# Kernel optimization log

Measured on AMD Instinct MI355X. Metric: run time of the kernel, lower is better.

The kernel has to match this reference:

```python
import jax, jax.numpy as jnp
import numpy as np

# Config (matches init_kwargs)
T, B = 128, 32
I, H, O, G = 128, 320, 32, 8
GROUP = 16  # attn_group_size entries, 8 groups of 16 -> sums to I
DT, TAU_X, TAU_W = 0.02, 0.1, 0.2
ALPHA_X = DT / TAU_X          # 0.2
ALPHA_W = DT / TAU_W          # 0.1
E_PROP = 0.8


def _masks():
    e_h = int(E_PROP * H)  # 256
    # x2h: e_prop=1, zero_cols_prop=0, no diag removal -> all ones
    mask_x = jnp.ones((H, I), dtype=jnp.float32)
    # h2h: sign mask (+1 for E, -1 for I), diagonal zeroed
    sign_h = jnp.concatenate([jnp.ones(e_h), -jnp.ones(H - e_h)]).astype(jnp.float32)
    mask_h = jnp.tile(sign_h[None, :], (H, 1)) * (1.0 - jnp.eye(H, dtype=jnp.float32))
    # h2o: zero_cols = int(0.2*H) trailing columns removed, sign mask on the rest
    zc = int((1.0 - E_PROP) * H)  # 64
    exist = jnp.concatenate([jnp.ones(H - zc), jnp.zeros(zc)]).astype(jnp.float32)
    mask_o = jnp.tile((sign_h * exist)[None, :], (O, 1))
    # attn EILinear(H -> G): same column pattern as h2o
    mask_a = jnp.tile((sign_h * exist)[None, :], (G, 1))
    return mask_x, mask_h, mask_o, mask_a


def setup_inputs() -> dict:
    key = jax.random.key(0)
    ks = jax.random.split(key, 10)
    s = 0.05  # keep dynamics in a sane range
    return {
        "x": jax.random.normal(ks[0], (T, B, I), dtype=jnp.float32),
        "Rs": jax.random.uniform(ks[1], (T, B, 1), dtype=jnp.float32),
        "W_x2h": jax.random.normal(ks[2], (H, I), dtype=jnp.float32) * s,
        "W_h2h": jax.random.normal(ks[3], (H, H), dtype=jnp.float32) * s,
        "b_h2h": jax.random.normal(ks[4], (H,), dtype=jnp.float32) * s,
        "W_h2o": jax.random.normal(ks[5], (O, H), dtype=jnp.float32) * s,
        "b_h2o": jax.random.normal(ks[6], (O,), dtype=jnp.float32) * s,
        "W_attn": jax.random.normal(ks[7], (G, H), dtype=jnp.float32) * s,
        "b_attn": jax.random.normal(ks[8], (G,), dtype=jnp.float32) * s,
        "c_plas": jax.random.normal(ks[9], (6,), dtype=jnp.float32) * s,
    }


def reference(x, Rs, W_x2h, W_h2h, b_h2h, W_h2o, b_h2o, W_attn, b_attn, c_plas):
    mask_x, mask_h, mask_o, mask_a = _masks()
    relu = jax.nn.relu
    # effective (sign/existence constrained, positive) weights
    ew_attn = relu(W_attn) * mask_a                      # [G, H]
    ew_x0 = relu(W_x2h) * mask_x                         # [H, I]
    ew_h0 = relu(W_h2h) * mask_h                         # [H, H]
    c = jnp.abs(c_plas)

    state0 = jnp.zeros((B, H), dtype=x.dtype)            # x0=0, sigma_rec=0
    output0 = relu(state0)
    wx0 = jnp.broadcast_to(ew_x0[None], (B, H, I))       # batched fast weights
    wh0 = jnp.broadcast_to(ew_h0[None], (B, H, H))

    def step(carry, inp):
        state, output, wx, wh = carry
        x_t, R_t = inp                                   # [B,I], [B,1]
        # attention over hidden groups
        attn = jax.nn.softmax(output @ ew_attn.T + b_attn, axis=-1)  # [B,G]
        attn_full = jnp.repeat(attn, GROUP, axis=-1)     # [B,I]
        xm = x_t * attn_full * G
        # masked / positive-constrained fast weights applied per batch
        ewx = relu(wx) * mask_x[None]                    # [B,H,I]
        ewh = relu(wh) * mask_h[None]                    # [B,H,H]
        total = (jnp.einsum('bhi,bi->bh', ewx, xm)
                 + jnp.einsum('bhj,bj->bh', ewh, output) + b_h2h)
        new_state = state * (1.0 - ALPHA_X) + total * ALPHA_X
        new_output = jnp.tanh(relu(new_state))           # retanh
        # outer-product plasticity update
        R = R_t[:, :, None]                              # [B,1,1]
        wx_n = wx * (1.0 - ALPHA_W) + ALPHA_W * R * (
            c[0] * xm[:, None, :]
            + c[1] * new_output[:, :, None]
            + c[2] * jnp.einsum('bi,bj->bij', new_output, xm))
        wh_n = wh * (1.0 - ALPHA_W) + ALPHA_W * R * (
            c[3] * output[:, None, :]
            + c[4] * new_output[:, :, None]
            + c[5] * jnp.einsum('bi,bj->bij', new_output, output))
        return (new_state, new_output, wx_n, wh_n), new_output

    _, hs = jax.lax.scan(step, (state0, output0, wx0, wh0), (x, Rs))  # hs: [T,B,H]
    ew_o = relu(W_h2o) * mask_o                          # [O,H]
    out = jax.nn.sigmoid(jnp.einsum('tbh,oh->tbo', hs, ew_o) + b_h2o)
    return out, hs
```

## Files before the change

kernel.cpp:

```cpp
#include <hip/hip_runtime.h>

#define TT 128
#define BB 32
#define II 128
#define HH 320
#define OO 32
#define GG 8
#define HPAD 129

static __device__ __forceinline__ float fexp2(float x) { return __builtin_amdgcn_exp2f(x); }
static __device__ __forceinline__ float frcp(float x)  { return __builtin_amdgcn_rcpf(x); }

static __device__ __forceinline__ float tanh_pos(float x) {
    float e = fexp2(x * 2.8853900817779268f);
    return 1.0f - 2.0f * frcp(e + 1.0f);
}

__global__ __launch_bounds__(512, 2)
void leaky_rnn_kernel(const float* __restrict__ x, const float* __restrict__ Rs,
                      const float* __restrict__ Wx2h, const float* __restrict__ Wh2h,
                      const float* __restrict__ bh2h, const float* __restrict__ Wh2o,
                      const float* __restrict__ bh2o, const float* __restrict__ Wattn,
                      const float* __restrict__ battn, const float* __restrict__ cplas,
                      float* __restrict__ out, float* __restrict__ hs,
                      unsigned* __restrict__ ctr)
{
    const int tid  = threadIdx.x;
    const int bid  = blockIdx.x;
    const int b    = bid >> 3;
    const int sub  = bid & 7;
    const int w    = tid >> 6;
    const int lane = tid & 63;
    const int h0   = sub * 40;

    __shared__ float s_ea[GG * HH];
    __shared__ float s_out[2][HH];
    __shared__ float s_logit[GG];
    __shared__ float s_hist[40 * HPAD];
    __shared__ float s_hs[16 * HH];

    for (int idx = tid; idx < GG * HH; idx += 512) {
        int h = idx % HH;
        float m = (h < 256) ? 1.f : (h == 256 ? -1.f : 0.f);
        s_ea[idx] = fmaxf(Wattn[idx], 0.f) * m;
    }
    if (tid < HH) { s_out[0][tid] = 0.f; s_out[1][tid] = 0.f; }

    float wx[5][2], wh[5][5], st[5], bh[5];
    int hrow[5];
#pragma unroll
    for (int r = 0; r < 5; ++r) {
        int h = h0 + w * 5 + r;
        hrow[r] = h;
        bh[r] = bh2h[h];
        st[r] = 0.f;
#pragma unroll
        for (int c = 0; c < 2; ++c)
            wx[r][c] = fmaxf(Wx2h[h * II + lane + 64 * c], 0.f);
#pragma unroll
        for (int c = 0; c < 5; ++c) {
            int j = lane + 64 * c;
            float v = fmaxf(Wh2h[h * HH + j], 0.f);
            v = (c == 4) ? -v : v;
            wh[r][c] = (j == h) ? 0.f : v;
        }
    }
    float batt = battn[w];
    float c0 = fabsf(cplas[0]), c1 = fabsf(cplas[1]), c2 = fabsf(cplas[2]);
    float c3 = fabsf(cplas[3]), c4 = fabsf(cplas[4]), c5 = fabsf(cplas[5]);

    const float AX  = (float)(0.02 / 0.1);
    const float AW  = (float)(0.02 / 0.2);
    const float OMX = 1.f - AX;
    const float OMW = 1.f - AW;
    const float L2E = 1.4426950408889634f;

    __syncthreads();

    float xv0n = x[b * II + lane];
    float xv1n = x[b * II + lane + 64];
    float Rvn  = Rs[b];

#pragma unroll 1
    for (int t = 0; t < TT; ++t) {
        const float* so_cur = s_out[t & 1];
        float*       so_nxt = s_out[(t + 1) & 1];
        float xv0 = xv0n, xv1 = xv1n;
        float A   = AW * Rvn;

        float lp = 0.f;
#pragma unroll
        for (int k = 0; k < 5; ++k) {
            int hh2 = lane + 64 * k;
            lp = fmaf(s_ea[w * HH + hh2], so_cur[hh2], lp);
        }
#pragma unroll
        for (int m = 1; m < 64; m <<= 1) lp += __shfl_xor(lp, m, 64);
        if (lane == 0) s_logit[w] = lp + batt;
        __syncthreads();

        float lg[8];
#pragma unroll
        for (int g = 0; g < 8; ++g) lg[g] = s_logit[g];
        float mx = lg[0];
#pragma unroll
        for (int g = 1; g < 8; ++g) mx = fmaxf(mx, lg[g]);
        float se = 0.f, eg[8];
#pragma unroll
        for (int g = 0; g < 8; ++g) { eg[g] = fexp2((lg[g] - mx) * L2E); se += eg[g]; }
        float rinv = frcp(se);
        float xmc0 = xv0 * eg[lane >> 4] * 8.f * rinv;
        float xmc1 = xv1 * eg[(lane >> 4) + 4] * 8.f * rinv;

        float oc[5];
#pragma unroll
        for (int c = 0; c < 5; ++c) oc[c] = so_cur[lane + 64 * c];

        float p[5];
#pragma unroll
        for (int r = 0; r < 5; ++r) {
            int h = hrow[r];
            float pp = fmaxf(wx[r][0], 0.f) * xmc0;
            pp = fmaf(fmaxf(wx[r][1], 0.f), xmc1, pp);
#pragma unroll
            for (int c = 0; c < 5; ++c) {
                float wv = fmaxf(wh[r][c], 0.f);
                float so = (c == 4) ? -oc[4] : oc[c];
                float term = wv * so;
                term = ((lane + 64 * c) == h) ? 0.f : term;
                pp += term;
            }
            p[r] = pp;
        }
#pragma unroll
        for (int m = 1; m < 64; m <<= 1) {
#pragma unroll
            for (int r = 0; r < 5; ++r) p[r] += __shfl_xor(p[r], m, 64);
        }

        float no[5];
#pragma unroll
        for (int r = 0; r < 5; ++r) {
            float total = p[r] + bh[r];
            st[r] = fmaf(st[r], OMX, total * AX);
            no[r] = tanh_pos(fmaxf(st[r], 0.f));
        }

        {
            float pub = no[0];
            pub = (lane == 1) ? no[1] : pub;
            pub = (lane == 2) ? no[2] : pub;
            pub = (lane == 3) ? no[3] : pub;
            pub = (lane == 4) ? no[4] : pub;
            if (lane < 5) {
                __hip_atomic_store(&hs[(t * BB + b) * HH + h0 + w * 5 + lane], pub + 2.0f,
                                   __ATOMIC_RELAXED, __HIP_MEMORY_SCOPE_AGENT);
                s_hist[(w * 5 + lane) * HPAD + t] = pub;
            }
        }

        if (t < TT - 1) {
            float Ac0 = A * c0, Ac1 = A * c1, Ac2 = A * c2;
            float Ac3 = A * c3, Ac4 = A * c4, Ac5 = A * c5;
#pragma unroll
            for (int r = 0; r < 5; ++r) {
                float u  = fmaf(Ac2, no[r], Ac0);
                float v  = Ac1 * no[r];
                float pp = fmaf(Ac5, no[r], Ac3);
                float qq = Ac4 * no[r];
                wx[r][0] = fmaf(wx[r][0], OMW, fmaf(u, xmc0, v));
                wx[r][1] = fmaf(wx[r][1], OMW, fmaf(u, xmc1, v));
#pragma unroll
                for (int c = 0; c < 5; ++c)
                    wh[r][c] = fmaf(wh[r][c], OMW, fmaf(pp, oc[c], qq));
            }
        }

        if (t + 1 < TT) {
            xv0n = x[((t + 1) * BB + b) * II + lane];
            xv1n = x[((t + 1) * BB + b) * II + lane + 64];
            Rvn  = Rs[(t + 1) * BB + b];
        }

        if (t < TT - 1 && tid < HH) {
            const float* p2 = &hs[(t * BB + b) * HH + tid];
            float v; int guard = 0;
            do {
                v = __hip_atomic_load(p2, __ATOMIC_RELAXED, __HIP_MEMORY_SCOPE_AGENT);
            } while (v < 1.0f && ++guard < 2000000);
            so_nxt[tid] = v - 2.0f;
        }
        __syncthreads();
    }

    if (tid == 0) {
        __hip_atomic_fetch_add(&ctr[b * 32], 1u, __ATOMIC_RELAXED, __HIP_MEMORY_SCOPE_AGENT);
        int guard = 0;
        while (__hip_atomic_load(&ctr[b * 32], __ATOMIC_RELAXED, __HIP_MEMORY_SCOPE_AGENT) < 8u) {
            if (++guard > 2000000) break;
            __builtin_amdgcn_s_sleep(1);
        }
    }
    __syncthreads();

    for (int idx = tid; idx < 16 * HH; idx += 512) {
        int tl = idx / HH, h = idx % HH;
        int t_g = sub * 16 + tl;
        s_hs[idx] = __hip_atomic_load(&hs[(t_g * BB + b) * HH + h],
                                      __ATOMIC_RELAXED, __HIP_MEMORY_SCOPE_AGENT) - 2.0f;
    }
    __syncthreads();
    {
        int t_loc = tid >> 5;
        int o     = tid & 31;
        int t_g   = sub * 16 + t_loc;
        const float* hp = &s_hs[t_loc * HH];
        float acc = bh2o[o];
#pragma unroll 4
        for (int h = 0; h < 257; ++h) {
            float m = (h == 256) ? -1.f : 1.f;
            acc = fmaf(fmaxf(Wh2o[o * HH + h], 0.f) * m, hp[h], acc);
        }
        float sg = frcp(1.f + fexp2(-acc * L2E));
        out[(t_g * BB + b) * OO + o] = sg;
    }

    __syncthreads();
    if (tid == 0) {
        __hip_atomic_fetch_add(&ctr[b * 32], 1u, __ATOMIC_RELAXED, __HIP_MEMORY_SCOPE_AGENT);
        int guard = 0;
        while (__hip_atomic_load(&ctr[b * 32], __ATOMIC_RELAXED, __HIP_MEMORY_SCOPE_AGENT) < 16u) {
            if (++guard > 2000000) break;
            __builtin_amdgcn_s_sleep(1);
        }
    }
    __syncthreads();

    for (int idx = tid; idx < 40 * TT; idx += 512) {
        int row = idx >> 7;
        int t   = idx & 127;
        __hip_atomic_store(&hs[(t * BB + b) * HH + h0 + row], s_hist[row * HPAD + t],
                           __ATOMIC_RELAXED, __HIP_MEMORY_SCOPE_AGENT);
    }
}

extern "C" void kernel_launch(void* const* d_in, const int* in_sizes, int n_in,
                              void* d_out, int out_size, void* d_ws, size_t ws_size,
                              hipStream_t stream) {
    const float* x     = (const float*)d_in[0];
    const float* Rs    = (const float*)d_in[1];
    const float* Wx2h  = (const float*)d_in[2];
    const float* Wh2h  = (const float*)d_in[3];
    const float* bh2h  = (const float*)d_in[4];
    const float* Wh2o  = (const float*)d_in[5];
    const float* bh2o  = (const float*)d_in[6];
    const float* Wattn = (const float*)d_in[7];
    const float* battn = (const float*)d_in[8];
    const float* cplas = (const float*)d_in[9];
    float* out = (float*)d_out;
    float* hs  = out + TT * BB * OO;
    unsigned* ctr = (unsigned*)d_ws;

    hipMemsetAsync(d_ws, 0, 32 * 32 * sizeof(unsigned), stream);
    hipLaunchKernelGGL(leaky_rnn_kernel, dim3(256), dim3(512), 0, stream,
                       x, Rs, Wx2h, Wh2h, bh2h, Wh2o, bh2o, Wattn, battn, cplas,
                       out, hs, ctr);
}
```

Baseline: 476.7 us.

## Remove per-step block barriers by keeping hidden state and attention weights in registers

Each wave now polls the full previous hidden vector straight from global memory into registers, so the shared-memory hidden buffer and both __syncthreads per timestep are gone. Every wave computes all eight attention logits itself from register-resident attention weights, using batched shuffle reductions instead of one logit per wave passed through shared memory. This removes barrier latency on the serial recurrence critical path. In exchange it adds redundant logit arithmetic, more shuffles, more register pressure under the 512-thread, 2-block launch bound, and five times as many polling loads per step.

```diff
diff --git a/kernel.cpp b/kernel.cpp
--- a/kernel.cpp
+++ b/kernel.cpp
@@ -33,18 +33,20 @@
     const int lane = tid & 63;
     const int h0   = sub * 40;
 
-    __shared__ float s_ea[GG * HH];
-    __shared__ float s_out[2][HH];
-    __shared__ float s_logit[GG];
     __shared__ float s_hist[40 * HPAD];
     __shared__ float s_hs[16 * HH];
 
-    for (int idx = tid; idx < GG * HH; idx += 512) {
-        int h = idx % HH;
-        float m = (h < 256) ? 1.f : (h == 256 ? -1.f : 0.f);
-        s_ea[idx] = fmaxf(Wattn[idx], 0.f) * m;
-    }
-    if (tid < HH) { s_out[0][tid] = 0.f; s_out[1][tid] = 0.f; }
+    float ea_r[8][5], ba[8];
+#pragma unroll
+    for (int g = 0; g < 8; ++g) {
+        ba[g] = battn[g];
+#pragma unroll
+        for (int k = 0; k < 5; ++k) {
+            int j = lane + 64 * k;
+            float m = (j < 256) ? 1.f : (j == 256 ? -1.f : 0.f);
+            ea_r[g][k] = fmaxf(Wattn[g * HH + j], 0.f) * m;
+        }
+    }
 
     float wx[5][2], wh[5][5], st[5], bh[5];
     int hrow[5];
@@ -65,7 +67,6 @@
             wh[r][c] = (j == h) ? 0.f : v;
         }
     }
-    float batt = battn[w];
     float c0 = fabsf(cplas[0]), c1 = fabsf(cplas[1]), c2 = fabsf(cplas[2]);
     float c3 = fabsf(cplas[3]), c4 = fabsf(cplas[4]), c5 = fabsf(cplas[5]);
 
@@ -75,7 +76,7 @@
     const float OMW = 1.f - AW;
     const float L2E = 1.4426950408889634f;
 
-    __syncthreads();
+    float oc[5] = {0.f, 0.f, 0.f, 0.f, 0.f};
 
     float xv0n = x[b * II + lane];
     float xv1n = x[b * II + lane + 64];
@@ -83,25 +84,26 @@
 
 #pragma unroll 1
     for (int t = 0; t < TT; ++t) {
-        const float* so_cur = s_out[t & 1];
-        float*       so_nxt = s_out[(t + 1) & 1];
         float xv0 = xv0n, xv1 = xv1n;
         float A   = AW * Rvn;
 
-        float lp = 0.f;
-#pragma unroll
-        for (int k = 0; k < 5; ++k) {
-            int hh2 = lane + 64 * k;
-            lp = fmaf(s_ea[w * HH + hh2], so_cur[hh2], lp);
-        }
-#pragma unroll
-        for (int m = 1; m < 64; m <<= 1) lp += __shfl_xor(lp, m, 64);
-        if (lane == 0) s_logit[w] = lp + batt;
-        __syncthreads();
-
         float lg[8];
 #pragma unroll
-        for (int g = 0; g < 8; ++g) lg[g] = s_logit[g];
+        for (int g = 0; g < 8; ++g) {
+            float lp = 0.f;
+#pragma unroll
+            for (int k = 0; k < 5; ++k)
+                lp = fmaf(ea_r[g][k], oc[k], lp);
+            lg[g] = lp;
+        }
+#pragma unroll
+        for (int m = 1; m < 64; m <<= 1) {
+#pragma unroll
+            for (int g = 0; g < 8; ++g) lg[g] += __shfl_xor(lg[g], m, 64);
+        }
+#pragma unroll
+        for (int g = 0; g < 8; ++g) lg[g] += ba[g];
+
         float mx = lg[0];
 #pragma unroll
         for (int g = 1; g < 8; ++g) mx = fmaxf(mx, lg[g]);
@@ -111,10 +113,6 @@
         float rinv = frcp(se);
         float xmc0 = xv0 * eg[lane >> 4] * 8.f * rinv;
         float xmc1 = xv1 * eg[(lane >> 4) + 4] * 8.f * rinv;
-
-        float oc[5];
-#pragma unroll
-        for (int c = 0; c < 5; ++c) oc[c] = so_cur[lane + 64 * c];
 
         float p[5];
 #pragma unroll
@@ -182,16 +180,25 @@
             Rvn  = Rs[(t + 1) * BB + b];
         }
 
-        if (t < TT - 1 && tid < HH) {
-            const float* p2 = &hs[(t * BB + b) * HH + tid];
-            float v; int guard = 0;
+        if (t < TT - 1) {
+            const float* base = &hs[(t * BB + b) * HH + lane];
+            float v0, v1, v2, v3, v4;
+            int guard = 0;
             do {
-                v = __hip_atomic_load(p2, __ATOMIC_RELAXED, __HIP_MEMORY_SCOPE_AGENT);
-            } while (v < 1.0f && ++guard < 2000000);
-            so_nxt[tid] = v - 2.0f;
-        }
-        __syncthreads();
-    }
+                v0 = __hip_atomic_load(base,       __ATOMIC_RELAXED, __HIP_MEMORY_SCOPE_AGENT);
+                v1 = __hip_atomic_load(base + 64,  __ATOMIC_RELAXED, __HIP_MEMORY_SCOPE_AGENT);
+                v2 = __hip_atomic_load(base + 128, __ATOMIC_RELAXED, __HIP_MEMORY_SCOPE_AGENT);
+                v3 = __hip_atomic_load(base + 192, __ATOMIC_RELAXED, __HIP_MEMORY_SCOPE_AGENT);
+                v4 = __hip_atomic_load(base + 256, __ATOMIC_RELAXED, __HIP_MEMORY_SCOPE_AGENT);
+                float mn = fminf(fminf(fminf(v0, v1), fminf(v2, v3)), v4);
+                if (mn >= 1.0f) break;
+            } while (++guard < 2000000);
+            oc[0] = v0 - 2.0f; oc[1] = v1 - 2.0f; oc[2] = v2 - 2.0f;
+            oc[3] = v3 - 2.0f; oc[4] = v4 - 2.0f;
+        }
+    }
+
+    __syncthreads();
 
     if (tid == 0) {
         __hip_atomic_fetch_add(&ctr[b * 32], 1u, __ATOMIC_RELAXED, __HIP_MEMORY_SCOPE_AGENT);
```

Measured after the change: 577.4 us. 21.1% more time.

## Interleave two batch elements per block to hide cross-block exchange latency

Applied to the files above, without the earlier changes.

Each block now processes two batch elements, alternating their recurrent steps so that the global-memory spin-wait for one batch's hidden state overlaps with computing the other batch's step. The grid is halved to 128 blocks. Entries the block produced itself are read from local shared history instead of polling global memory. In exchange, register pressure doubles (two sets of plastic weights per thread), which may cause spills under the 512x2 launch bounds. The per-block serial work also doubles.

```diff
diff --git a/kernel.cpp b/kernel.cpp
--- a/kernel.cpp
+++ b/kernel.cpp
@@ -27,16 +27,20 @@
 {
     const int tid  = threadIdx.x;
     const int bid  = blockIdx.x;
-    const int b    = bid >> 3;
+    const int pair = bid >> 3;
     const int sub  = bid & 7;
+    const int bA   = pair * 2;
+    const int bB   = bA + 1;
     const int w    = tid >> 6;
     const int lane = tid & 63;
     const int h0   = sub * 40;
 
     __shared__ float s_ea[GG * HH];
-    __shared__ float s_out[2][HH];
-    __shared__ float s_logit[GG];
-    __shared__ float s_hist[40 * HPAD];
+    __shared__ float s_outA[HH];
+    __shared__ float s_outB[HH];
+    __shared__ float s_logit[2][GG];
+    __shared__ float s_histA[40 * HPAD];
+    __shared__ float s_histB[40 * HPAD];
     __shared__ float s_hs[16 * HH];
 
     for (int idx = tid; idx < GG * HH; idx += 512) {
@@ -44,25 +48,30 @@
         float m = (h < 256) ? 1.f : (h == 256 ? -1.f : 0.f);
         s_ea[idx] = fmaxf(Wattn[idx], 0.f) * m;
     }
-    if (tid < HH) { s_out[0][tid] = 0.f; s_out[1][tid] = 0.f; }
-
-    float wx[5][2], wh[5][5], st[5], bh[5];
+    if (tid < HH) { s_outA[tid] = 0.f; s_outB[tid] = 0.f; }
+
+    float wxA[5][2], whA[5][5], stA[5];
+    float wxB[5][2], whB[5][5], stB[5];
+    float bh[5];
     int hrow[5];
 #pragma unroll
     for (int r = 0; r < 5; ++r) {
         int h = h0 + w * 5 + r;
         hrow[r] = h;
         bh[r] = bh2h[h];
-        st[r] = 0.f;
-#pragma unroll
-        for (int c = 0; c < 2; ++c)
-            wx[r][c] = fmaxf(Wx2h[h * II + lane + 64 * c], 0.f);
+        stA[r] = 0.f; stB[r] = 0.f;
+#pragma unroll
+        for (int c = 0; c < 2; ++c) {
+            float v = fmaxf(Wx2h[h * II + lane + 64 * c], 0.f);
+            wxA[r][c] = v; wxB[r][c] = v;
+        }
 #pragma unroll
         for (int c = 0; c < 5; ++c) {
             int j = lane + 64 * c;
             float v = fmaxf(Wh2h[h * HH + j], 0.f);
             v = (c == 4) ? -v : v;
-            wh[r][c] = (j == h) ? 0.f : v;
+            v = (j == h) ? 0.f : v;
+            whA[r][c] = v; whB[r][c] = v;
         }
     }
     float batt = battn[w];
@@ -77,160 +86,286 @@
 
     __syncthreads();
 
-    float xv0n = x[b * II + lane];
-    float xv1n = x[b * II + lane + 64];
-    float Rvn  = Rs[b];
+    float xA0n = x[bA * II + lane];
+    float xA1n = x[bA * II + lane + 64];
+    float xB0n = x[bB * II + lane];
+    float xB1n = x[bB * II + lane + 64];
+    float RvAn = Rs[bA];
+    float RvBn = Rs[bB];
 
 #pragma unroll 1
     for (int t = 0; t < TT; ++t) {
-        const float* so_cur = s_out[t & 1];
-        float*       so_nxt = s_out[(t + 1) & 1];
-        float xv0 = xv0n, xv1 = xv1n;
-        float A   = AW * Rvn;
-
-        float lp = 0.f;
-#pragma unroll
-        for (int k = 0; k < 5; ++k) {
-            int hh2 = lane + 64 * k;
-            lp = fmaf(s_ea[w * HH + hh2], so_cur[hh2], lp);
-        }
-#pragma unroll
-        for (int m = 1; m < 64; m <<= 1) lp += __shfl_xor(lp, m, 64);
-        if (lane == 0) s_logit[w] = lp + batt;
-        __syncthreads();
-
-        float lg[8];
-#pragma unroll
-        for (int g = 0; g < 8; ++g) lg[g] = s_logit[g];
-        float mx = lg[0];
-#pragma unroll
-        for (int g = 1; g < 8; ++g) mx = fmaxf(mx, lg[g]);
-        float se = 0.f, eg[8];
-#pragma unroll
-        for (int g = 0; g < 8; ++g) { eg[g] = fexp2((lg[g] - mx) * L2E); se += eg[g]; }
-        float rinv = frcp(se);
-        float xmc0 = xv0 * eg[lane >> 4] * 8.f * rinv;
-        float xmc1 = xv1 * eg[(lane >> 4) + 4] * 8.f * rinv;
-
-        float oc[5];
-#pragma unroll
-        for (int c = 0; c < 5; ++c) oc[c] = so_cur[lane + 64 * c];
-
-        float p[5];
-#pragma unroll
-        for (int r = 0; r < 5; ++r) {
-            int h = hrow[r];
-            float pp = fmaxf(wx[r][0], 0.f) * xmc0;
-            pp = fmaf(fmaxf(wx[r][1], 0.f), xmc1, pp);
-#pragma unroll
-            for (int c = 0; c < 5; ++c) {
-                float wv = fmaxf(wh[r][c], 0.f);
-                float so = (c == 4) ? -oc[4] : oc[c];
-                float term = wv * so;
-                term = ((lane + 64 * c) == h) ? 0.f : term;
-                pp += term;
-            }
-            p[r] = pp;
-        }
-#pragma unroll
-        for (int m = 1; m < 64; m <<= 1) {
-#pragma unroll
-            for (int r = 0; r < 5; ++r) p[r] += __shfl_xor(p[r], m, 64);
-        }
-
-        float no[5];
-#pragma unroll
-        for (int r = 0; r < 5; ++r) {
-            float total = p[r] + bh[r];
-            st[r] = fmaf(st[r], OMX, total * AX);
-            no[r] = tanh_pos(fmaxf(st[r], 0.f));
-        }
+        const float AA = AW * RvAn;
+        const float AB = AW * RvBn;
 
         {
+            float lp = 0.f;
+#pragma unroll
+            for (int k = 0; k < 5; ++k) {
+                int hh2 = lane + 64 * k;
+                lp = fmaf(s_ea[w * HH + hh2], s_outA[hh2], lp);
+            }
+#pragma unroll
+            for (int m = 1; m < 64; m <<= 1) lp += __shfl_xor(lp, m, 64);
+            if (lane == 0) s_logit[0][w] = lp + batt;
+        }
+        __syncthreads();
+        {
+            float lg[8];
+#pragma unroll
+            for (int g = 0; g < 8; ++g) lg[g] = s_logit[0][g];
+            float mx = lg[0];
+#pragma unroll
+            for (int g = 1; g < 8; ++g) mx = fmaxf(mx, lg[g]);
+            float se = 0.f, eg[8];
+#pragma unroll
+            for (int g = 0; g < 8; ++g) { eg[g] = fexp2((lg[g] - mx) * L2E); se += eg[g]; }
+            float rinv = frcp(se);
+            float xmc0 = xA0n * eg[lane >> 4] * 8.f * rinv;
+            float xmc1 = xA1n * eg[(lane >> 4) + 4] * 8.f * rinv;
+
+            float oc[5];
+#pragma unroll
+            for (int c = 0; c < 5; ++c) oc[c] = s_outA[lane + 64 * c];
+
+            float p[5];
+#pragma unroll
+            for (int r = 0; r < 5; ++r) {
+                int h = hrow[r];
+                float pp = fmaxf(wxA[r][0], 0.f) * xmc0;
+                pp = fmaf(fmaxf(wxA[r][1], 0.f), xmc1, pp);
+#pragma unroll
+                for (int c = 0; c < 5; ++c) {
+                    float wv = fmaxf(whA[r][c], 0.f);
+                    float so = (c == 4) ? -oc[4] : oc[c];
+                    float term = wv * so;
+                    term = ((lane + 64 * c) == h) ? 0.f : term;
+                    pp += term;
+                }
+                p[r] = pp;
+            }
+#pragma unroll
+            for (int m = 1; m < 64; m <<= 1) {
+#pragma unroll
+                for (int r = 0; r < 5; ++r) p[r] += __shfl_xor(p[r], m, 64);
+            }
+
+            float no[5];
+#pragma unroll
+            for (int r = 0; r < 5; ++r) {
+                float total = p[r] + bh[r];
+                stA[r] = fmaf(stA[r], OMX, total * AX);
+                no[r] = tanh_pos(fmaxf(stA[r], 0.f));
+            }
+
             float pub = no[0];
             pub = (lane == 1) ? no[1] : pub;
             pub = (lane == 2) ? no[2] : pub;
             pub = (lane == 3) ? no[3] : pub;
             pub = (lane == 4) ? no[4] : pub;
             if (lane < 5) {
-                __hip_atomic_store(&hs[(t * BB + b) * HH + h0 + w * 5 + lane], pub + 2.0f,
+                __hip_atomic_store(&hs[(t * BB + bA) * HH + h0 + w * 5 + lane], pub + 2.0f,
                                    __ATOMIC_RELAXED, __HIP_MEMORY_SCOPE_AGENT);
-                s_hist[(w * 5 + lane) * HPAD + t] = pub;
-            }
-        }
-
-        if (t < TT - 1) {
-            float Ac0 = A * c0, Ac1 = A * c1, Ac2 = A * c2;
-            float Ac3 = A * c3, Ac4 = A * c4, Ac5 = A * c5;
+                s_histA[(w * 5 + lane) * HPAD + t] = pub;
+            }
+
+            if (t < TT - 1) {
+                float Ac0 = AA * c0, Ac1 = AA * c1, Ac2 = AA * c2;
+                float Ac3 = AA * c3, Ac4 = AA * c4, Ac5 = AA * c5;
+#pragma unroll
+                for (int r = 0; r < 5; ++r) {
+                    float u  = fmaf(Ac2, no[r], Ac0);
+                    float v  = Ac1 * no[r];
+                    float pq = fmaf(Ac5, no[r], Ac3);
+                    float qq = Ac4 * no[r];
+                    wxA[r][0] = fmaf(wxA[r][0], OMW, fmaf(u, xmc0, v));
+                    wxA[r][1] = fmaf(wxA[r][1], OMW, fmaf(u, xmc1, v));
+#pragma unroll
+                    for (int c = 0; c < 5; ++c)
+                        whA[r][c] = fmaf(whA[r][c], OMW, fmaf(pq, oc[c], qq));
+                }
+            }
+        }
+
+        if (t > 0 && tid < HH) {
+            float v;
+            if (tid >= h0 && tid < h0 + 40) {
+                v = s_histB[(tid - h0) * HPAD + (t - 1)];
+            } else {
+                const float* p2 = &hs[((t - 1) * BB + bB) * HH + tid];
+                int guard = 0;
+                do {
+                    v = __hip_atomic_load(p2, __ATOMIC_RELAXED, __HIP_MEMORY_SCOPE_AGENT);
+                    if (++guard > 2000000) break;
+                } while (v < 1.0f);
+                v -= 2.0f;
+            }
+            s_outB[tid] = v;
+        }
+        __syncthreads();
+
+        {
+            float lp = 0.f;
+#pragma unroll
+            for (int k = 0; k < 5; ++k) {
+                int hh2 = lane + 64 * k;
+                lp = fmaf(s_ea[w * HH + hh2], s_outB[hh2], lp);
+            }
+#pragma unroll
+            for (int m = 1; m < 64; m <<= 1) lp += __shfl_xor(lp, m, 64);
+            if (lane == 0) s_logit[1][w] = lp + batt;
+        }
+        __syncthreads();
+        {
+            float lg[8];
+#pragma unroll
+            for (int g = 0; g < 8; ++g) lg[g] = s_logit[1][g];
+            float mx = lg[0];
+#pragma unroll
+            for (int g = 1; g < 8; ++g) mx = fmaxf(mx, lg[g]);
+            float se = 0.f, eg[8];
+#pragma unroll
+            for (int g = 0; g < 8; ++g) { eg[g] = fexp2((lg[g] - mx) * L2E); se += eg[g]; }
+            float rinv = frcp(se);
+            float xmc0 = xB0n * eg[lane >> 4] * 8.f * rinv;
+            float xmc1 = xB1n * eg[(lane >> 4) + 4] * 8.f * rinv;
+
+            float oc[5];
+#pragma unroll
+            for (int c = 0; c < 5; ++c) oc[c] = s_outB[lane + 64 * c];
+
+            float p[5];
 #pragma unroll
             for (int r = 0; r < 5; ++r) {
-                float u  = fmaf(Ac2, no[r], Ac0);
-                float v  = Ac1 * no[r];
-                float pp = fmaf(Ac5, no[r], Ac3);
-                float qq = Ac4 * no[r];
-                wx[r][0] = fmaf(wx[r][0], OMW, fmaf(u, xmc0, v));
-                wx[r][1] = fmaf(wx[r][1], OMW, fmaf(u, xmc1, v));
-#pragma unroll
-                for (int c = 0; c < 5; ++c)
-                    wh[r][c] = fmaf(wh[r][c], OMW, fmaf(pp, oc[c], qq));
+                int h = hrow[r];
+                float pp = fmaxf(wxB[r][0], 0.f) * xmc0;
+                pp = fmaf(fmaxf(wxB[r][1], 0.f), xmc1, pp);
+#pragma unroll
+                for (int c = 0; c < 5; ++c) {
+                    float wv = fmaxf(whB[r][c], 0.f);
+                    float so = (c == 4) ? -oc[4] : oc[c];
+                    float term = wv * so;
+                    term = ((lane + 64 * c) == h) ? 0.f : term;
+                    pp += term;
+                }
+                p[r] = pp;
+            }
+#pragma unroll
+            for (int m = 1; m < 64; m <<= 1) {
+#pragma unroll
+                for (int r = 0; r < 5; ++r) p[r] += __shfl_xor(p[r], m, 64);
+            }
+
+            float no[5];
+#pragma unroll
+            for (int r = 0; r < 5; ++r) {
+                float total = p[r] + bh[r];
+                stB[r] = fmaf(stB[r], OMX, total * AX);
+                no[r] = tanh_pos(fmaxf(stB[r], 0.f));
+            }
+
+            float pub = no[0];
+            pub = (lane == 1) ? no[1] : pub;
+            pub = (lane == 2) ? no[2] : pub;
+            pub = (lane == 3) ? no[3] : pub;
+            pub = (lane == 4) ? no[4] : pub;
+            if (lane < 5) {
+                __hip_atomic_store(&hs[(t * BB + bB) * HH + h0 + w * 5 + lane], pub + 2.0f,
+                                   __ATOMIC_RELAXED, __HIP_MEMORY_SCOPE_AGENT);
+                s_histB[(w * 5 + lane) * HPAD + t] = pub;
+            }
+
+            if (t < TT - 1) {
+                float Ac0 = AB * c0, Ac1 = AB * c1, Ac2 = AB * c2;
+                float Ac3 = AB * c3, Ac4 = AB * c4, Ac5 = AB * c5;
+#pragma unroll
+                for (int r = 0; r < 5; ++r) {
+                    float u  = fmaf(Ac2, no[r], Ac0);
+                    float v  = Ac1 * no[r];
+                    float pq = fmaf(Ac5, no[r], Ac3);
+                    float qq = Ac4 * no[r];
+                    wxB[r][0] = fmaf(wxB[r][0], OMW, fmaf(u, xmc0, v));
+                    wxB[r][1] = fmaf(wxB[r][1], OMW, fmaf(u, xmc1, v));
+#pragma unroll
+                    for (int c = 0; c < 5; ++c)
+                        whB[r][c] = fmaf(whB[r][c], OMW, fmaf(pq, oc[c], qq));
+                }
             }
         }
 
         if (t + 1 < TT) {
-            xv0n = x[((t + 1) * BB + b) * II + lane];
-            xv1n = x[((t + 1) * BB + b) * II + lane + 64];
-            Rvn  = Rs[(t + 1) * BB + b];
+            xA0n = x[((t + 1) * BB + bA) * II + lane];
+            xA1n = x[((t + 1) * BB + bA) * II + lane + 64];
+            xB0n = x[((t + 1) * BB + bB) * II + lane];
+            xB1n = x[((t + 1) * BB + bB) * II + lane + 64];
+            RvAn = Rs[(t + 1) * BB + bA];
+            RvBn = Rs[(t + 1) * BB + bB];
         }
 
         if (t < TT - 1 && tid < HH) {
-            const float* p2 = &hs[(t * BB + b) * HH + tid];
-            float v; int guard = 0;
-            do {
-                v = __hip_atomic_load(p2, __ATOMIC_RELAXED, __HIP_MEMORY_SCOPE_AGENT);
-            } while (v < 1.0f && ++guard < 2000000);
-            so_nxt[tid] = v - 2.0f;
+            float v;
+            if (tid >= h0 && tid < h0 + 40) {
+                v = s_histA[(tid - h0) * HPAD + t];
+            } else {
+                const float* p2 = &hs[(t * BB + bA) * HH + tid];
+                int guard = 0;
+                do {
+                    v = __hip_atomic_load(p2, __ATOMIC_RELAXED, __HIP_MEMORY_SCOPE_AGENT);
+                    if (++guard > 2000000) break;
+                } while (v < 1.0f);
+                v -= 2.0f;
+            }
+            s_outA[tid] = v;
         }
         __syncthreads();
     }
 
     if (tid == 0) {
-        __hip_atomic_fetch_add(&ctr[b * 32], 1u, __ATOMIC_RELAXED, __HIP_MEMORY_SCOPE_AGENT);
+        __hip_atomic_fetch_add(&ctr[bA * 32], 1u, __ATOMIC_RELAXED, __HIP_MEMORY_SCOPE_AGENT);
+        __hip_atomic_fetch_add(&ctr[bB * 32], 1u, __ATOMIC_RELAXED, __HIP_MEMORY_SCOPE_AGENT);
         int guard = 0;
-        while (__hip_atomic_load(&ctr[b * 32], __ATOMIC_RELAXED, __HIP_MEMORY_SCOPE_AGENT) < 8u) {
-            if (++guard > 2000000) break;
+        while (__hip_atomic_load(&ctr[bA * 32], __ATOMIC_RELAXED, __HIP_MEMORY_SCOPE_AGENT) < 8u ||
+               __hip_atomic_load(&ctr[bB * 32], __ATOMIC_RELAXED, __HIP_MEMORY_SCOPE_AGENT) < 8u) {
+            if (++guard > 4000000) break;
             __builtin_amdgcn_s_sleep(1);
         }
     }
     __syncthreads();
 
-    for (int idx = tid; idx < 16 * HH; idx += 512) {
-        int tl = idx / HH, h = idx % HH;
-        int t_g = sub * 16 + tl;
-        s_hs[idx] = __hip_atomic_load(&hs[(t_g * BB + b) * HH + h],
-                                      __ATOMIC_RELAXED, __HIP_MEMORY_SCOPE_AGENT) - 2.0f;
-    }
-    __syncthreads();
-    {
-        int t_loc = tid >> 5;
-        int o     = tid & 31;
-        int t_g   = sub * 16 + t_loc;
-        const float* hp = &s_hs[t_loc * HH];
-        float acc = bh2o[o];
+#pragma unroll 1
+    for (int pass = 0; pass < 2; ++pass) {
+        const int bb = pass ? bB : bA;
+        for (int idx = tid; idx < 16 * HH; idx += 512) {
+            int tl = idx / HH, h = idx % HH;
+            int t_g = sub * 16 + tl;
+            s_hs[idx] = __hip_atomic_load(&hs[(t_g * BB + bb) * HH + h],
+                                          __ATOMIC_RELAXED, __HIP_MEMORY_SCOPE_AGENT) - 2.0f;
+        }
+        __syncthreads();
+        {
+            int t_loc = tid >> 5;
+            int o     = tid & 31;
+            int t_g   = sub * 16 + t_loc;
+            const float* hp = &s_hs[t_loc * HH];
+            float acc = bh2o[o];
 #pragma unroll 4
-        for (int h = 0; h < 257; ++h) {
-            float m = (h == 256) ? -1.f : 1.f;
-            acc = fmaf(fmaxf(Wh2o[o * HH + h], 0.f) * m, hp[h], acc);
-        }
-        float sg = frcp(1.f + fexp2(-acc * L2E));
-        out[(t_g * BB + b) * OO + o] = sg;
-    }
-
-    __syncthreads();
+            for (int h = 0; h < 257; ++h) {
+                float m = (h == 256) ? -1.f : 1.f;
+                acc = fmaf(fmaxf(Wh2o[o * HH + h], 0.f) * m, hp[h], acc);
+            }
+            float sg = frcp(1.f + fexp2(-acc * L2E));
+            out[(t_g * BB + bb) * OO + o] = sg;
+        }
+        __syncthreads();
+    }
+
     if (tid == 0) {
-        __hip_atomic_fetch_add(&ctr[b * 32], 1u, __ATOMIC_RELAXED, __HIP_MEMORY_SCOPE_AGENT);
+        __hip_atomic_fetch_add(&ctr[bA * 32], 1u, __ATOMIC_RELAXED, __HIP_MEMORY_SCOPE_AGENT);
+        __hip_atomic_fetch_add(&ctr[bB * 32], 1u, __ATOMIC_RELAXED, __HIP_MEMORY_SCOPE_AGENT);
         int guard = 0;
-        while (__hip_atomic_load(&ctr[b * 32], __ATOMIC_RELAXED, __HIP_MEMORY_SCOPE_AGENT) < 16u) {
-            if (++guard > 2000000) break;
+        while (__hip_atomic_load(&ctr[bA * 32], __ATOMIC_RELAXED, __HIP_MEMORY_SCOPE_AGENT) < 16u ||
+               __hip_atomic_load(&ctr[bB * 32], __ATOMIC_RELAXED, __HIP_MEMORY_SCOPE_AGENT) < 16u) {
+            if (++guard > 4000000) break;
             __builtin_amdgcn_s_sleep(1);
         }
     }
@@ -239,7 +374,9 @@
     for (int idx = tid; idx < 40 * TT; idx += 512) {
         int row = idx >> 7;
         int t   = idx & 127;
-        __hip_atomic_store(&hs[(t * BB + b) * HH + h0 + row], s_hist[row * HPAD + t],
+        __hip_atomic_store(&hs[(t * BB + bA) * HH + h0 + row], s_histA[row * HPAD + t],
+                           __ATOMIC_RELAXED, __HIP_MEMORY_SCOPE_AGENT);
+        __hip_atomic_store(&hs[(t * BB + bB) * HH + h0 + row], s_histB[row * HPAD + t],
                            __ATOMIC_RELAXED, __HIP_MEMORY_SCOPE_AGENT);
     }
 }
@@ -262,7 +399,7 @@
     unsigned* ctr = (unsigned*)d_ws;
 
     hipMemsetAsync(d_ws, 0, 32 * 32 * sizeof(unsigned), stream);
-    hipLaunchKernelGGL(leaky_rnn_kernel, dim3(256), dim3(512), 0, stream,
+    hipLaunchKernelGGL(leaky_rnn_kernel, dim3(128), dim3(512), 0, stream,
                        x, Rs, Wx2h, Wh2h, bh2h, Wh2o, bh2o, Wattn, battn, cplas,
                        out, hs, ctr);
 }
```

Result: slower. 768.4 us (+61.2%).
